# Performance work log

Measured on AMD Instinct MI355X. Metric: run time of the kernel, lower is better.

## Reference

```python
import jax, jax.numpy as jnp
import numpy as np

# ---- static config (mirrors init_kwargs) ----
B, T, N, FIN = 32, 12, 500, 2
U, ND, ED = 32, 32, 2            # factor dim, node_dim, edge_dim
NRES, NDIL, NSKIP, NEND, NPRED = 32, 32, 256, 512, 12
NBLOCKS, NLAYERS, KS, ORDER = 4, 2, 2, 2
L = NBLOCKS * NLAYERS
DILATIONS = [2 ** i for _ in range(NBLOCKS) for i in range(NLAYERS)]
RF = NBLOCKS * (KS - 1) * (2 ** NLAYERS - 1) + 1  # receptive field = 13
GCIN = (ORDER * ED + 1) * NDIL                     # graph-conv concat channels = 160
BN_EPS = 1e-5


def conv1x1(x, w, b):
    # x: [B,C,N,T], w: [O,C]
    return jnp.einsum('bcnt,oc->bont', x, w) + b[None, :, None, None]


def dilated_tconv(x, w, b, d):
    # valid dilated conv along time. x: [B,C,N,T], w: [O,C,K]
    k_sz = w.shape[-1]
    t_out = x.shape[-1] - (k_sz - 1) * d
    out = jnp.einsum('bcnt,oc->bont', x[..., 0:t_out], w[..., 0])
    for k in range(1, k_sz):
        out = out + jnp.einsum('bcnt,oc->bont', x[..., k * d:k * d + t_out], w[..., k])
    return out + b[None, :, None, None]


def graph_conv(x, supports, w, b):
    # x: [B,C,N,T]; supports: [E,N,N]; diffusion over node axis (dim 2)
    out = [x]
    for e in range(supports.shape[0]):
        x1 = jnp.einsum('bcvt,vw->bcwt', x, supports[e])
        out.append(x1)
        for _ in range(ORDER - 1):
            x1 = jnp.einsum('bcvt,vw->bcwt', x1, supports[e])
            out.append(x1)
    h = jnp.concatenate(out, axis=1)  # [B,GCIN,N,T]
    return conv1x1(h, w, b)


def batchnorm(x, g, bta):
    m = x.mean(axis=(0, 2, 3), keepdims=True)
    v = ((x - m) ** 2).mean(axis=(0, 2, 3), keepdims=True)
    return (x - m) * jax.lax.rsqrt(v + BN_EPS) * g[None, :, None, None] + bta[None, :, None, None]


def _forward(inputs, factor, map_w, map_b, a1w, a1b, a2w, a2b, a3w, a3b,
             enter_w, enter_b, filt_w, filt_b, gate_w, gate_b,
             skp_w, skp_b, gc_w, gc_b, bn_g, bn_b, o1w, o1b, o2w, o2b):
    n = factor.shape[0]
    # ---- adaptive supports ----
    v = jax.nn.relu(factor @ map_w + map_b)                      # [N, ND]
    src = jnp.broadcast_to(v[None, :, :], (n, n, v.shape[1]))    # src[i,j]=v[j]
    dst = jnp.broadcast_to(v[:, None, :], (n, n, v.shape[1]))    # dst[i,j]=v[i]
    h = jnp.concatenate([src, dst], axis=-1)                     # [N,N,2*ND]
    h = jax.nn.relu(h @ a1w + a1b)
    h = jax.nn.relu(h @ a2w + a2b)
    adj = (h @ a3w + a3b).transpose(2, 0, 1)                     # [E,N,N]
    adj = jax.nn.softmax(adj, axis=2)
    supports = jnp.maximum(adj, jnp.eye(n, dtype=adj.dtype))
    # ---- input split ----
    static = jnp.einsum('btuf,pu->btpf', jnp.einsum('btnf,nu->btuf', inputs, factor), factor)
    x = jnp.concatenate([static, inputs - static], axis=-1)      # [B,T,N,2F]
    x = x.transpose(0, 3, 2, 1)                                  # [B,2F,N,T]
    t_in = x.shape[-1]
    if t_in < RF:
        x = jnp.pad(x, ((0, 0), (0, 0), (0, 0), (RF - t_in, 0)))
    x = conv1x1(x, enter_w, enter_b)                             # [B,NRES,N,RF]
    skip = jnp.zeros((x.shape[0], NSKIP, n, x.shape[-1]), dtype=x.dtype)
    # ---- stacked ST layers ----
    for i, d in enumerate(DILATIONS):
        residual = x
        f = jnp.tanh(dilated_tconv(x, filt_w[i], filt_b[i], d))
        g = jax.nn.sigmoid(dilated_tconv(x, gate_w[i], gate_b[i], d))
        x = f * g                                                # [B,NDIL,N,T']
        s = conv1x1(x, skp_w[i], skp_b[i])
        skip = skip[..., skip.shape[-1] - s.shape[-1]:] + s
        x = graph_conv(x, supports, gc_w[i], gc_b[i])
        x = x + residual[..., residual.shape[-1] - x.shape[-1]:]
        x = batchnorm(x, bn_g[i], bn_b[i])
    # ---- output head ----
    y = jax.nn.relu(skip)
    y = jax.nn.relu(conv1x1(y, o1w, o1b))
    y = conv1x1(y, o2w, o2b)                                     # [B,NPRED,N,1]
    return y, supports


def setup_inputs() -> dict:
    key = jax.random.key(0)
    ks = jax.random.split(key, 16)
    def w(i, shape, s=0.02):
        return s * jax.random.normal(ks[i], shape, dtype=jnp.float32)
    return {
        'inputs': jax.random.normal(ks[0], (B, T, N, FIN), dtype=jnp.float32),
        'factor': 0.05 * jax.random.normal(ks[1], (N, U), dtype=jnp.float32),
        'map_w': w(2, (U, ND), 0.1), 'map_b': jnp.zeros((ND,), jnp.float32),
        'a1w': w(3, (2 * ND, 2 * ND), 0.1), 'a1b': jnp.zeros((2 * ND,), jnp.float32),
        'a2w': w(4, (2 * ND, ND), 0.1), 'a2b': jnp.zeros((ND,), jnp.float32),
        'a3w': w(5, (ND, ED), 0.1), 'a3b': jnp.zeros((ED,), jnp.float32),
        'enter_w': w(6, (NRES, 2 * FIN)), 'enter_b': jnp.zeros((NRES,), jnp.float32),
        'filt_w': w(7, (L, NDIL, NRES, KS)), 'filt_b': jnp.zeros((L, NDIL), jnp.float32),
        'gate_w': w(8, (L, NDIL, NRES, KS)), 'gate_b': jnp.zeros((L, NDIL), jnp.float32),
        'skp_w': w(9, (L, NSKIP, NDIL)), 'skp_b': jnp.zeros((L, NSKIP), jnp.float32),
        'gc_w': w(10, (L, NRES, GCIN)), 'gc_b': jnp.zeros((L, NRES), jnp.float32),
        'bn_g': jnp.ones((L, NRES), jnp.float32), 'bn_b': jnp.zeros((L, NRES), jnp.float32),
        'o1w': w(11, (NEND, NSKIP)), 'o1b': jnp.zeros((NEND,), jnp.float32),
        'o2w': w(12, (NPRED, NEND)), 'o2b': jnp.zeros((NPRED,), jnp.float32),
    }


def reference(inputs, factor, map_w, map_b, a1w, a1b, a2w, a2b, a3w, a3b,
              enter_w, enter_b, filt_w, filt_b, gate_w, gate_b,
              skp_w, skp_b, gc_w, gc_b, bn_g, bn_b, o1w, o1b, o2w, o2b):
    return _forward(inputs, factor, map_w, map_b, a1w, a1b, a2w, a2b, a3w, a3b,
                    enter_w, enter_b, filt_w, filt_b, gate_w, gate_b,
                    skp_w, skp_b, gc_w, gc_b, bn_g, bn_b, o1w, o1b, o2w, o2b)
```

## Files before the change

### kernel.cpp

```cpp
#include <hip/hip_runtime.h>
#include <math.h>

#define BB 32
#define TT 12
#define NN 500
#define UU 32
#define CC 32
#define NSKIPC 256
#define NENDC 512
#define NPREDC 12
#define TX 13
#define TG 12
#define QS 384
#define VS 512
#define BNN (BB*NN)
#define DSZ (BNN*TG*CC)
#define BN_EPS 1e-5f

#define OFF_V      0u
#define OFF_ADJ    16000u
#define OFF_ASRC   516000u
#define OFF_ADST   548000u
#define OFF_PROJ   580000u
#define OFF_STAT   582048u
#define OFF_PART   582560u
#define OFF_BSUM   774560u
#define OFF_X      774816u
#define OFF_XN     7430816u
#define OFF_D      14086816u
#define OFF_GBF    38662816u
#define OFF_GLB    41734816u
#define OFF_GT     43782816u
#define OFF_ST     46928544u
#define OFF_SB     47190688u
#define OFF_ST2    47452832u
#define OFF_WSTB   47714976u
#define OFF_O1WB   47747744u
#define OFF_SKV    47813280u
#define OFF_Y1B    49861280u

typedef __attribute__((ext_vector_type(8))) short bf16x8;
typedef __attribute__((ext_vector_type(4))) float f32x4;

__device__ inline unsigned short f2bf(float f) {
  union { float f; unsigned u; } x; x.f = f;
  unsigned r = x.u + 0x7FFFu + ((x.u >> 16) & 1u);
  return (unsigned short)(r >> 16);
}
__device__ inline float bf2f(short s) {
  union { float f; unsigned u; } x;
  x.u = ((unsigned)(unsigned short)s) << 16;
  return x.f;
}
__device__ inline int pk2(float a, float b) {
  return (int)((unsigned)f2bf(a) | ((unsigned)f2bf(b) << 16));
}
__device__ inline bf16x8 pack8(f32x4 a, f32x4 b) {
  union { int i[4]; bf16x8 v; } u;
  u.i[0]=pk2(a.x,a.y); u.i[1]=pk2(a.z,a.w);
  u.i[2]=pk2(b.x,b.y); u.i[3]=pk2(b.z,b.w);
  return u.v;
}
__device__ inline f32x4 reluadd(f32x4 a, f32x4 b) {
  f32x4 r;
  r.x=fmaxf(a.x+b.x,0.f); r.y=fmaxf(a.y+b.y,0.f);
  r.z=fmaxf(a.z+b.z,0.f); r.w=fmaxf(a.w+b.w,0.f);
  return r;
}


__global__ void k_v(const float* __restrict__ factor, const float* __restrict__ map_w,
                    const float* __restrict__ map_b, float* __restrict__ v) {
  int n = blockIdx.x; int d = threadIdx.x;
  __shared__ float fr[UU];
  fr[d] = factor[n*UU + d];
  __syncthreads();
  float acc = map_b[d];
#pragma unroll
  for (int u=0;u<UU;u++) acc += fr[u]*map_w[u*32+d];
  v[n*32+d] = fmaxf(acc, 0.f);
}

__global__ void k_asrc2(const float* __restrict__ v, const float* __restrict__ a1w,
                        const float* __restrict__ a1b,
                        float* __restrict__ asrc, float* __restrict__ adst) {
  int n = blockIdx.x; int o = threadIdx.x;
  __shared__ float vn[32];
  if (o < 32) vn[o] = v[n*32+o];
  __syncthreads();
  float s = 0.f, dst = a1b[o];
#pragma unroll
  for (int u=0;u<32;u++){ s += vn[u]*a1w[u*64+o]; dst += vn[u]*a1w[(32+u)*64+o]; }
  asrc[n*64+o] = s;
  adst[n*64+o] = dst;
}

__global__ __launch_bounds__(256) void k_pair3(const float* __restrict__ asrc,
    const float* __restrict__ adst, const float* __restrict__ a2w,
    const float* __restrict__ a2b, const float* __restrict__ a3w,
    const float* __restrict__ a3b, float* __restrict__ adj) {
  int i = blockIdx.x;
  int tid = threadIdx.x;
  int wid = tid>>6, lane = tid&63;
  int lm = lane&15, g = lane>>4, lk8 = g*8;
  int jb = blockIdx.y*256 + wid*64;
  bf16x8 wf[2][2];
#pragma unroll
  for (int ks=0;ks<2;ks++)
#pragma unroll
    for (int nh=0;nh<2;nh++){
      int n = nh*16+lm;
      f32x4 lo, hi;
      lo.x=a2w[(ks*32+lk8+0)*32+n]; lo.y=a2w[(ks*32+lk8+1)*32+n];
      lo.z=a2w[(ks*32+lk8+2)*32+n]; lo.w=a2w[(ks*32+lk8+3)*32+n];
      hi.x=a2w[(ks*32+lk8+4)*32+n]; hi.y=a2w[(ks*32+lk8+5)*32+n];
      hi.z=a2w[(ks*32+lk8+6)*32+n]; hi.w=a2w[(ks*32+lk8+7)*32+n];
      wf[ks][nh] = pack8(lo, hi);
    }
  float b20 = a2b[lm], b21 = a2b[16+lm];
  float w3e0n0 = a3w[lm*2],      w3e1n0 = a3w[lm*2+1];
  float w3e0n1 = a3w[(16+lm)*2], w3e1n1 = a3w[(16+lm)*2+1];
  float b30 = a3b[0], b31 = a3b[1];
  const float* dp = adst + i*64;
  f32x4 d00 = *(const f32x4*)(dp + lk8);
  f32x4 d01 = *(const f32x4*)(dp + lk8 + 4);
  f32x4 d10 = *(const f32x4*)(dp + 32 + lk8);
  f32x4 d11 = *(const f32x4*)(dp + 32 + lk8 + 4);
#pragma unroll
  for (int mg=0; mg<4; mg++){
    int j = jb + mg*16 + lm;
    int jc = j < 500 ? j : 0;
    const float* ap = asrc + jc*64;
    f32x4 s00=*(const f32x4*)(ap+lk8),    s01=*(const f32x4*)(ap+lk8+4);
    f32x4 s10=*(const f32x4*)(ap+32+lk8), s11=*(const f32x4*)(ap+32+lk8+4);
    bf16x8 a0 = pack8(reluadd(s00,d00), reluadd(s01,d01));
    bf16x8 a1 = pack8(reluadd(s10,d10), reluadd(s11,d11));
    f32x4 acc0 = {b20,b20,b20,b20};
    f32x4 acc1 = {b21,b21,b21,b21};
    acc0 = __builtin_amdgcn_mfma_f32_16x16x32_bf16(a0, wf[0][0], acc0, 0,0,0);
    acc0 = __builtin_amdgcn_mfma_f32_16x16x32_bf16(a1, wf[1][0], acc0, 0,0,0);
    acc1 = __builtin_amdgcn_mfma_f32_16x16x32_bf16(a0, wf[0][1], acc1, 0,0,0);
    acc1 = __builtin_amdgcn_mfma_f32_16x16x32_bf16(a1, wf[1][1], acc1, 0,0,0);
    float e0[4], e1[4];
#pragma unroll
    for (int r=0;r<4;r++){
      float h2a = fmaxf(acc0[r],0.f), h2b = fmaxf(acc1[r],0.f);
      e0[r] = h2a*w3e0n0 + h2b*w3e0n1;
      e1[r] = h2a*w3e1n0 + h2b*w3e1n1;
    }
#pragma unroll
    for (int off=1; off<16; off<<=1){
#pragma unroll
      for (int r=0;r<4;r++){ e0[r]+=__shfl_xor(e0[r],off); e1[r]+=__shfl_xor(e1[r],off); }
    }
    if (lm==0){
      int j4 = jb + mg*16 + g*4;
      if (j4 < 500){
        f32x4 v0={e0[0]+b30,e0[1]+b30,e0[2]+b30,e0[3]+b30};
        f32x4 v1={e1[0]+b31,e1[1]+b31,e1[2]+b31,e1[3]+b31};
        *(f32x4*)(adj + i*500 + j4) = v0;
        *(f32x4*)(adj + 250000 + i*500 + j4) = v1;
      }
    }
  }
}

__global__ __launch_bounds__(256) void k_softmax(const float* __restrict__ adj,
    float* __restrict__ sup_out) {
  int row = blockIdx.x;
  int e = row/NN, i = row%NN;
  const float* a = adj + e*250000 + i*NN;
  __shared__ float red[64];
  float m = -1e30f;
  for (int j=threadIdx.x;j<NN;j+=256) m = fmaxf(m, a[j]);
#pragma unroll
  for (int off=32; off; off>>=1) m = fmaxf(m, __shfl_down(m, off));
  int lane = threadIdx.x & 63, wid = threadIdx.x >> 6;
  if (lane==0) red[wid]=m;
  __syncthreads();
  if (threadIdx.x==0){ float mm=red[0]; for(int w=1;w<4;w++) mm=fmaxf(mm,red[w]); red[32]=mm; }
  __syncthreads();
  m = red[32];
  float s=0.f;
  for (int j=threadIdx.x;j<NN;j+=256) s += __expf(a[j]-m);
#pragma unroll
  for (int off=32; off; off>>=1) s += __shfl_down(s, off);
  if (lane==0) red[wid]=s;
  __syncthreads();
  if (threadIdx.x==0){ float ss=0; for(int w=0;w<4;w++) ss+=red[w]; red[33]=ss; }
  __syncthreads();
  float inv = 1.f/red[33];
  for (int j=threadIdx.x;j<NN;j+=256) {
    float val = __expf(a[j]-m)*inv;
    if (j==i) val = 1.f;
    sup_out[e*250000 + i*NN + j] = val;
  }
}

__global__ __launch_bounds__(256) void k_tposeS(const float* __restrict__ sup,
    short* __restrict__ ST, short* __restrict__ SB) {
  __shared__ float ts[64][68];
  int e = blockIdx.z;
  int v0 = blockIdx.x*64, w0 = blockIdx.y*64;
  int tid = threadIdx.x;
  int vv = tid>>2, wc = (tid&3)*16;
  bool vok = (v0+vv) < 500;
#pragma unroll
  for (int c=0;c<4;c++){
    f32x4 val = {0,0,0,0};
    int wg = w0 + wc + c*4;
    if (vok && wg < 500) val = *(const f32x4*)(sup + e*250000 + (size_t)(v0+vv)*500 + wg);
    *(f32x4*)&ts[vv][wc + c*4] = val;
    int2 pv; pv.x = pk2(val.x, val.y); pv.y = pk2(val.z, val.w);
    *(int2*)(SB + (size_t)e*(512*512) + (size_t)(v0+vv)*VS + wg) = pv;
  }
  __syncthreads();
  int w = tid>>2, vc = (tid&3)*16;
  unsigned short u[16];
#pragma unroll
  for (int j=0;j<16;j++) u[j] = f2bf(ts[vc+j][w]);
  int4 o0, o1;
  o0.x = u[0]|(u[1]<<16);  o0.y = u[2]|(u[3]<<16);
  o0.z = u[4]|(u[5]<<16);  o0.w = u[6]|(u[7]<<16);
  o1.x = u[8]|(u[9]<<16);  o1.y = u[10]|(u[11]<<16);
  o1.z = u[12]|(u[13]<<16); o1.w = u[14]|(u[15]<<16);
  short* op = ST + (size_t)e*(512*512) + (size_t)(w0+w)*VS + v0 + vc;
  *(int4*)(op) = o0;
  *(int4*)(op+8) = o1;
}

__global__ __launch_bounds__(256) void k_ssq(const short* __restrict__ SB,
    const short* __restrict__ ST, short* __restrict__ ST2) {
  __shared__ __align__(16) short As[64*72];
  __shared__ __align__(16) short Bs[64*72];
  int e = blockIdx.z;
  int u0 = blockIdx.x*64, w0 = blockIdx.y*64;
  const short* Ab = SB + (size_t)e*(512*512);
  const short* Bb = ST + (size_t)e*(512*512);
  int tid = threadIdx.x;
  int row = tid>>2, col = (tid&3)*16;
  const short* ap = Ab + (size_t)(u0+row)*VS + col;
  const short* bp = Bb + (size_t)(w0+row)*VS + col;
  f32x4 ra0 = *(const f32x4*)(ap);
  f32x4 ra1 = *(const f32x4*)(ap+8);
  f32x4 rb0 = *(const f32x4*)(bp);
  f32x4 rb1 = *(const f32x4*)(bp+8);
  int wid = tid>>6, lane = tid&63;
  int wr = wid>>1, wc = wid&1;
  int lm = lane&15, lk = (lane>>4)*8;
  f32x4 acc[2][2] = {};
  short* aw = As + row*72 + col;
  short* bw = Bs + row*72 + col;
  for (int kk=0; kk<8; kk++) {
    __syncthreads();
    *(f32x4*)(aw) = ra0; *(f32x4*)(aw+8) = ra1;
    *(f32x4*)(bw) = rb0; *(f32x4*)(bw+8) = rb1;
    __syncthreads();
    if (kk < 7) {
      const short* ap2 = ap + (kk+1)*64;
      const short* bp2 = bp + (kk+1)*64;
      ra0 = *(const f32x4*)(ap2); ra1 = *(const f32x4*)(ap2+8);
      rb0 = *(const f32x4*)(bp2); rb1 = *(const f32x4*)(bp2+8);
    }
#pragma unroll
    for (int ks=0; ks<2; ks++) {
      bf16x8 af0 = *(const bf16x8*)(As + (wr*32 + lm)*72 + ks*32 + lk);
      bf16x8 af1 = *(const bf16x8*)(As + (wr*32 + 16 + lm)*72 + ks*32 + lk);
      bf16x8 bq0 = *(const bf16x8*)(Bs + (wc*32 + lm)*72 + ks*32 + lk);
      bf16x8 bq1 = *(const bf16x8*)(Bs + (wc*32 + 16 + lm)*72 + ks*32 + lk);
      acc[0][0] = __builtin_amdgcn_mfma_f32_16x16x32_bf16(af0, bq0, acc[0][0], 0,0,0);
      acc[0][1] = __builtin_amdgcn_mfma_f32_16x16x32_bf16(af0, bq1, acc[0][1], 0,0,0);
      acc[1][0] = __builtin_amdgcn_mfma_f32_16x16x32_bf16(af1, bq0, acc[1][0], 0,0,0);
      acc[1][1] = __builtin_amdgcn_mfma_f32_16x16x32_bf16(af1, bq1, acc[1][1], 0,0,0);
    }
  }
#pragma unroll
  for (int fm=0; fm<2; fm++) {
    int u4 = u0 + wr*32 + fm*16 + (lane>>4)*4;
#pragma unroll
    for (int fn=0; fn<2; fn++) {
      int w = w0 + wc*32 + fn*16 + lm;
      f32x4 v4 = acc[fm][fn];
      int2 pv; pv.x = pk2(v4.x, v4.y); pv.y = pk2(v4.z, v4.w);
      *(int2*)(ST2 + (size_t)e*(512*512) + (size_t)w*VS + u4) = pv;
    }
  }
}

__global__ __launch_bounds__(256) void k_tposeGb(const short* __restrict__ Gbf,
    short* __restrict__ GT, int qmax) {
  __shared__ __align__(16) short ts[64][72];
  int b = blockIdx.z;
  int v0 = blockIdx.x*64, q0 = blockIdx.y*64;
  int tid = threadIdx.x;
  int vv = tid>>2, qc = (tid&3)*16;
  bool ok = ((v0+vv) < 500) && ((q0+qc) < qmax);
  int4 z4 = {0,0,0,0};
  int4 i0 = z4, i1 = z4;
  if (ok){
    const short* gp = Gbf + (size_t)(b*NN + v0+vv)*QS + q0 + qc;
    i0 = *(const int4*)(gp);
    i1 = *(const int4*)(gp+8);
  }
  *(int4*)&ts[vv][qc] = i0;
  *(int4*)&ts[vv][qc+8] = i1;
  __syncthreads();
  int q = tid>>2, vc = (tid&3)*16;
  if (q0 + q < qmax) {
    unsigned short u[16];
#pragma unroll
    for (int j=0;j<16;j++) u[j] = (unsigned short)ts[vc+j][q];
    int4 o0, o1;
    o0.x = u[0]|(u[1]<<16);  o0.y = u[2]|(u[3]<<16);
    o0.z = u[4]|(u[5]<<16);  o0.w = u[6]|(u[7]<<16);
    o1.x = u[8]|(u[9]<<16);  o1.y = u[10]|(u[11]<<16);
    o1.z = u[12]|(u[13]<<16); o1.w = u[14]|(u[15]<<16);
    short* op = GT + ((size_t)b*QS + q0+q)*VS + v0 + vc;
    *(int4*)(op) = o0;
    *(int4*)(op+8) = o1;
  }
}

__global__ __launch_bounds__(256) void k_hop2(const short* __restrict__ ST,
    const short* __restrict__ ST2, const short* __restrict__ GT,
    short* __restrict__ Dout, int qmax) {
  __shared__ __align__(16) short As[128*72];
  __shared__ __align__(16) short Bs[128*72];
  int sel = blockIdx.z & 3, b = blockIdx.z >> 2;
  int e = sel >> 1, hop = sel & 1;
  int w0 = blockIdx.x*128, q0 = blockIdx.y*128;
  const short* Ab = (hop ? ST2 : ST) + (size_t)e*(512*512) + (size_t)w0*VS;
  const short* Bb = GT + (size_t)b*(QS*VS) + (size_t)q0*VS;
  int tid = threadIdx.x;
  int row = tid>>2, col = (tid&3)*16;
  const short* ap0 = Ab + (size_t)row*VS + col;
  const short* ap1 = ap0 + (size_t)64*VS;
  const short* bp0 = Bb + (size_t)row*VS + col;
  const short* bp1 = bp0 + (size_t)64*VS;
  f32x4 a00=*(const f32x4*)ap0, a01=*(const f32x4*)(ap0+8);
  f32x4 a10=*(const f32x4*)ap1, a11=*(const f32x4*)(ap1+8);
  f32x4 b00=*(const f32x4*)bp0, b01=*(const f32x4*)(bp0+8);
  f32x4 b10=*(const f32x4*)bp1, b11=*(const f32x4*)(bp1+8);
  int wid = tid>>6, lane = tid&63;
  int wr = wid>>1, wc = wid&1;
  int lm = lane&15, lk = (lane>>4)*8;
  f32x4 acc[4][4] = {};
  short* aw0 = As + row*72 + col; short* aw1 = aw0 + 64*72;
  short* bw0 = Bs + row*72 + col; short* bw1 = bw0 + 64*72;
  for (int kk=0; kk<8; kk++) {
    __syncthreads();
    *(f32x4*)(aw0) = a00; *(f32x4*)(aw0+8) = a01;
    *(f32x4*)(aw1) = a10; *(f32x4*)(aw1+8) = a11;
    *(f32x4*)(bw0) = b00; *(f32x4*)(bw0+8) = b01;
    *(f32x4*)(bw1) = b10; *(f32x4*)(bw1+8) = b11;
    __syncthreads();
    if (kk < 7) {
      int o = (kk+1)*64;
      a00=*(const f32x4*)(ap0+o); a01=*(const f32x4*)(ap0+o+8);
      a10=*(const f32x4*)(ap1+o); a11=*(const f32x4*)(ap1+o+8);
      b00=*(const f32x4*)(bp0+o); b01=*(const f32x4*)(bp0+o+8);
      b10=*(const f32x4*)(bp1+o); b11=*(const f32x4*)(bp1+o+8);
    }
#pragma unroll
    for (int ks=0; ks<2; ks++) {
      bf16x8 af[4], bq[4];
#pragma unroll
      for (int fm=0;fm<4;fm++) af[fm] = *(const bf16x8*)(As + (wr*64+fm*16+lm)*72 + ks*32 + lk);
#pragma unroll
      for (int fn=0;fn<4;fn++) bq[fn] = *(const bf16x8*)(Bs + (wc*64+fn*16+lm)*72 + ks*32 + lk);
#pragma unroll
      for (int fm=0;fm<4;fm++)
#pragma unroll
        for (int fn=0;fn<4;fn++)
          acc[fm][fn] = __builtin_amdgcn_mfma_f32_16x16x32_bf16(af[fm], bq[fn], acc[fm][fn], 0,0,0);
    }
  }
  short* Ob = Dout + (size_t)sel*DSZ + (size_t)b*(NN*QS);
#pragma unroll
  for (int fm=0; fm<4; fm++) {
    int wb4 = w0 + wr*64 + fm*16 + (lane>>4)*4;
    if (wb4 >= 500) continue;
#pragma unroll
    for (int fn=0; fn<4; fn++) {
      int q = q0 + wc*64 + fn*16 + lm;
      if (q < qmax) {
        f32x4 v4 = acc[fm][fn];
        short* op = Ob + (size_t)wb4*QS + q;
        op[0*QS] = (short)f2bf(v4.x);
        op[1*QS] = (short)f2bf(v4.y);
        op[2*QS] = (short)f2bf(v4.z);
        op[3*QS] = (short)f2bf(v4.w);
      }
    }
  }
}


__global__ void k_proj(const float* __restrict__ inputs, const float* __restrict__ factor,
                       float* __restrict__ proj) {
  int bt = blockIdx.x;
  __shared__ float xin[NN*2];
  for (int idx=threadIdx.x; idx<NN*2; idx+=64) xin[idx] = inputs[bt*NN*2 + idx];
  __syncthreads();
  int u = threadIdx.x>>1, f = threadIdx.x&1;
  float acc=0.f;
  for (int n=0;n<NN;n++) acc += xin[n*2+f]*factor[n*UU+u];
  proj[bt*64 + u*2+f] = acc;
}

__global__ __launch_bounds__(256) void k_enter(const float* __restrict__ inputs,
    const float* __restrict__ factor, const float* __restrict__ proj,
    const float* __restrict__ ew, const float* __restrict__ eb, float* __restrict__ X) {
  int idx = blockIdx.x*256+threadIdx.x;
  if (idx >= BB*NN*TX) return;
  int t = idx % TX; int n = (idx/TX)%NN; int b = idx/(TX*NN);
  float x4[4]={0.f,0.f,0.f,0.f};
  if (t>0) {
    int tt=t-1;
    float s0=0.f,s1=0.f;
    const float* pr = proj + (b*TT+tt)*64;
    const float* fr = factor + n*UU;
#pragma unroll
    for(int u=0;u<UU;u++){ s0 += pr[u*2]*fr[u]; s1 += pr[u*2+1]*fr[u]; }
    float i0 = inputs[((b*TT+tt)*NN+n)*2];
    float i1 = inputs[((b*TT+tt)*NN+n)*2+1];
    x4[0]=s0; x4[1]=s1; x4[2]=i0-s0; x4[3]=i1-s1;
  }
  float* xp = X + ((size_t)(b*NN+n)*TX + t)*CC;
#pragma unroll
  for(int o=0;o<CC;o++){
    xp[o] = eb[o] + ew[o*4]*x4[0] + ew[o*4+1]*x4[1] + ew[o*4+2]*x4[2] + ew[o*4+3]*x4[3];
  }
}


__global__ __launch_bounds__(256) void k_gated3(const float* __restrict__ X,
    short* __restrict__ Gbf, short* __restrict__ Glb,
    const float* __restrict__ fw, const float* __restrict__ fb,
    const float* __restrict__ gw, const float* __restrict__ gb,
    const float* __restrict__ stat, int use_stat, int d, int t_out, int lidx) {
  __shared__ __align__(16) short As[64*72];
  __shared__ __align__(16) short Wb[64*72];
  __shared__ float scs[32], shs[32];
  int tid = threadIdx.x;
  if (tid < 32) {
    scs[tid] = use_stat ? stat[tid] : 1.0f;
    shs[tid] = use_stat ? stat[32 + tid] : 0.0f;
  }
  for (int i = tid; i < 2048; i += 256) {
    int o = i >> 6, k = i & 63;
    Wb[o*72 + k]      = (short)f2bf(fw[i]);
    Wb[(32+o)*72 + k] = (short)f2bf(gw[i]);
  }
  __syncthreads();
  int m0 = blockIdx.x * 64;
  {
    int mm = tid & 63;
    int kb = (tid >> 6) * 16;
    int c0 = kb >> 1;
    int m = m0 + mm;
    int bn = m / t_out, t = m - bn * t_out;
    const float* xr = X + (size_t)bn * (TX * CC);
    float4 a0 = *(const float4*)(xr + t * 32 + c0);
    float4 a1 = *(const float4*)(xr + t * 32 + c0 + 4);
    float4 b0 = *(const float4*)(xr + (t + d) * 32 + c0);
    float4 b1 = *(const float4*)(xr + (t + d) * 32 + c0 + 4);
    float va[8] = {a0.x,a0.y,a0.z,a0.w,a1.x,a1.y,a1.z,a1.w};
    float vb[8] = {b0.x,b0.y,b0.z,b0.w,b1.x,b1.y,b1.z,b1.w};
    int iv[8];
#pragma unroll
    for (int j = 0; j < 8; j++) {
      float sc = scs[c0+j], sh = shs[c0+j];
      iv[j] = pk2(va[j]*sc + sh, vb[j]*sc + sh);
    }
    int4 w0 = {iv[0],iv[1],iv[2],iv[3]};
    int4 w1 = {iv[4],iv[5],iv[6],iv[7]};
    *(int4*)(As + mm*72 + kb) = w0;
    *(int4*)(As + mm*72 + kb + 8) = w1;
  }
  __syncthreads();
  int wid = tid>>6, lane = tid&63;
  int lm = lane&15, g = lane>>4, lk8 = g*8;
  f32x4 acc[4] = {};
#pragma unroll
  for (int kk=0; kk<2; kk++){
    bf16x8 af = *(const bf16x8*)(As + (wid*16+lm)*72 + kk*32 + lk8);
#pragma unroll
    for (int fn=0; fn<4; fn++){
      bf16x8 bq = *(const bf16x8*)(Wb + (fn*16+lm)*72 + kk*32 + lk8);
      acc[fn] = __builtin_amdgcn_mfma_f32_16x16x32_bf16(af, bq, acc[fn], 0,0,0);
    }
  }
#pragma unroll
  for (int fn=0; fn<2; fn++){
    int o = fn*16 + lm;
    float fbv = fb[o], gbv = gb[o];
#pragma unroll
    for (int r=0; r<4; r++){
      int m = m0 + wid*16 + g*4 + r;
      int bn = m / t_out, t = m - bn*t_out;
      float f = acc[fn][r] + fbv;
      float gg = acc[fn+2][r] + gbv;
      float th = 2.f/(1.f+__expf(-2.f*f)) - 1.f;
      float sg = 1.f/(1.f+__expf(-gg));
      unsigned short ov = f2bf(th*sg);
      Gbf[(size_t)bn*QS + t*32 + o] = (short)ov;
      if (t == t_out-1) Glb[(size_t)bn*256 + lidx*32 + o] = (short)ov;
    }
  }
}


template<int TOUT>
__global__ __launch_bounds__(256) void k_gc3(const short* __restrict__ Gbf,
    const short* __restrict__ Dbf, const float* __restrict__ Xc, float* __restrict__ Xn,
    const float* __restrict__ gcw, const float* __restrict__ gcb,
    const float* __restrict__ stat, int use_stat, float* __restrict__ part, int d) {
  int tid = threadIdx.x;
  int wid = tid>>6, lane = tid&63;
  int lm = lane&15, g = lane>>4, lk8 = g*8;
  int m0 = blockIdx.x*256 + wid*64;
  const int M = 16000*TOUT;
  float* pp = part + ((size_t)blockIdx.x*4 + wid)*64;
  if (m0 >= M){
    if (lane < 16){ pp[lane]=0.f; pp[16+lane]=0.f; pp[32+lane]=0.f; pp[48+lane]=0.f; }
    return;
  }
  bf16x8 wf[5][2];
#pragma unroll
  for (int ks=0;ks<5;ks++)
#pragma unroll
    for (int nh=0;nh<2;nh++){
      const float* wp = gcw + (nh*16+lm)*160 + ks*32 + lk8;
      wf[ks][nh] = pack8(*(const f32x4*)wp, *(const f32x4*)(wp+4));
    }
  float scn0 = use_stat ? stat[lm]    : 1.f;
  float scn1 = use_stat ? stat[16+lm] : 1.f;
  float shn0 = use_stat ? stat[32+lm] : 0.f;
  float shn1 = use_stat ? stat[48+lm] : 0.f;
  float gb0 = gcb[lm], gb1 = gcb[16+lm];
  float ss0=0.f, sq0=0.f, ss1=0.f, sq1=0.f;
#pragma unroll
  for (int mg=0; mg<4; mg++){
    int m = m0 + mg*16 + lm;
    int bn = m / TOUT; int t = m - bn*TOUT;
    size_t off = (size_t)bn*(TG*CC) + t*32 + lk8;
    f32x4 acc0={0,0,0,0}, acc1={0,0,0,0};
    {
      bf16x8 af = *(const bf16x8*)(Gbf + off);
      acc0 = __builtin_amdgcn_mfma_f32_16x16x32_bf16(af, wf[0][0], acc0, 0,0,0);
      acc1 = __builtin_amdgcn_mfma_f32_16x16x32_bf16(af, wf[0][1], acc1, 0,0,0);
    }
#pragma unroll
    for (int ks=1;ks<5;ks++){
      bf16x8 af = *(const bf16x8*)(Dbf + (size_t)(ks-1)*DSZ + off);
      acc0 = __builtin_amdgcn_mfma_f32_16x16x32_bf16(af, wf[ks][0], acc0, 0,0,0);
      acc1 = __builtin_amdgcn_mfma_f32_16x16x32_bf16(af, wf[ks][1], acc1, 0,0,0);
    }
#pragma unroll
    for (int r=0;r<4;r++){
      int mr = m0 + mg*16 + g*4 + r;
      int bnr = mr / TOUT; int tr = mr - bnr*TOUT;
      size_t xoff = (size_t)bnr*(TX*CC);
      float r0 = Xc[xoff + (tr+d)*32 + lm];
      float r1 = Xc[xoff + (tr+d)*32 + 16 + lm];
      float v0 = acc0[r] + gb0 + r0*scn0 + shn0;
      float v1 = acc1[r] + gb1 + r1*scn1 + shn1;
      Xn[xoff + tr*32 + lm] = v0;
      Xn[xoff + tr*32 + 16 + lm] = v1;
      ss0+=v0; sq0+=v0*v0; ss1+=v1; sq1+=v1*v1;
    }
  }
#pragma unroll
  for (int off=16; off<64; off<<=1){
    ss0+=__shfl_xor(ss0,off); sq0+=__shfl_xor(sq0,off);
    ss1+=__shfl_xor(ss1,off); sq1+=__shfl_xor(sq1,off);
  }
  if (lane<16){
    pp[lane]=ss0; pp[16+lane]=ss1; pp[32+lane]=sq0; pp[48+lane]=sq1;
  }
}

__global__ __launch_bounds__(64) void k_stat2a(const float* __restrict__ part, int nblk,
    float* __restrict__ part2) {
  int t = threadIdx.x;
  float s = 0.f;
  for (int i = blockIdx.x; i < nblk; i += 64) s += part[(size_t)i*64 + t];
  part2[blockIdx.x*64 + t] = s;
}

__global__ __launch_bounds__(64) void k_stat2b(const float* __restrict__ part2,
    const float* __restrict__ g, const float* __restrict__ b,
    float* __restrict__ statout, float cntinv) {
  int t = threadIdx.x;
  float s = 0.f;
#pragma unroll 8
  for (int i = 0; i < 64; i++) s += part2[i*64 + t];
  __shared__ float red[64];
  red[t] = s;
  __syncthreads();
  if (t < 32){
    float sum = red[t], sq = red[32+t];
    float m = sum*cntinv, var = sq*cntinv - m*m;
    float sc = rsqrtf(var + BN_EPS)*g[t];
    statout[t] = sc;
    statout[32+t] = b[t] - m*sc;
  }
}


__global__ void k_wstack2(const float* __restrict__ skp_w, const float* __restrict__ skp_b,
                          const float* __restrict__ o1w,
                          short* __restrict__ Wstb, short* __restrict__ o1wb,
                          float* __restrict__ bsum) {
  int bid = blockIdx.x;
  int idx = bid*256 + threadIdx.x;
  if (bid < 256){
    int kk = idx >> 8, o = idx & 255;
    Wstb[o*256 + kk] = (short)f2bf(skp_w[(kk>>5)*8192 + o*32 + (kk&31)]);
    if (idx < 256){
      float s=0.f;
      for (int l=0;l<8;l++) s += skp_b[l*256+idx];
      bsum[idx]=s;
    }
  } else {
    int j = idx - 65536;
    o1wb[j] = (short)f2bf(o1w[j]);
  }
}

__global__ __launch_bounds__(256) void k_mm(const short* __restrict__ A,
    const short* __restrict__ B, const float* __restrict__ bias,
    short* __restrict__ out, int ldout, int K) {
  __shared__ __align__(16) short As[64*72];
  __shared__ __align__(16) short Bs[64*72];
  int m0 = blockIdx.x*64, n0 = blockIdx.y*64;
  int tid = threadIdx.x;
  int row = tid>>2, col = (tid&3)*16;
  const short* ap = A + (size_t)(m0+row)*K + col;
  const short* bp = B + (size_t)(n0+row)*K + col;
  f32x4 ra0 = *(const f32x4*)(ap);
  f32x4 ra1 = *(const f32x4*)(ap+8);
  f32x4 rb0 = *(const f32x4*)(bp);
  f32x4 rb1 = *(const f32x4*)(bp+8);
  int wid = tid>>6, lane = tid&63;
  int wr = wid>>1, wc = wid&1;
  int lm = lane&15, lk = (lane>>4)*8;
  f32x4 acc[2][2] = {};
  short* aw = As + row*72 + col;
  short* bw = Bs + row*72 + col;
  int nk = K>>6;
  for (int kk=0; kk<nk; kk++) {
    __syncthreads();
    *(f32x4*)(aw) = ra0; *(f32x4*)(aw+8) = ra1;
    *(f32x4*)(bw) = rb0; *(f32x4*)(bw+8) = rb1;
    __syncthreads();
    if (kk < nk-1) {
      const short* ap2 = ap + (kk+1)*64;
      const short* bp2 = bp + (kk+1)*64;
      ra0 = *(const f32x4*)(ap2); ra1 = *(const f32x4*)(ap2+8);
      rb0 = *(const f32x4*)(bp2); rb1 = *(const f32x4*)(bp2+8);
    }
#pragma unroll
    for (int ks=0; ks<2; ks++) {
      bf16x8 af0 = *(const bf16x8*)(As + (wr*32 + lm)*72 + ks*32 + lk);
      bf16x8 af1 = *(const bf16x8*)(As + (wr*32 + 16 + lm)*72 + ks*32 + lk);
      bf16x8 bq0 = *(const bf16x8*)(Bs + (wc*32 + lm)*72 + ks*32 + lk);
      bf16x8 bq1 = *(const bf16x8*)(Bs + (wc*32 + 16 + lm)*72 + ks*32 + lk);
      acc[0][0] = __builtin_amdgcn_mfma_f32_16x16x32_bf16(af0, bq0, acc[0][0], 0,0,0);
      acc[0][1] = __builtin_amdgcn_mfma_f32_16x16x32_bf16(af0, bq1, acc[0][1], 0,0,0);
      acc[1][0] = __builtin_amdgcn_mfma_f32_16x16x32_bf16(af1, bq0, acc[1][0], 0,0,0);
      acc[1][1] = __builtin_amdgcn_mfma_f32_16x16x32_bf16(af1, bq1, acc[1][1], 0,0,0);
    }
  }
#pragma unroll
  for (int fm=0; fm<2; fm++) {
    int mb = m0 + wr*32 + fm*16 + (lane>>4)*4;
#pragma unroll
    for (int fn=0; fn<2; fn++) {
      int n = n0 + wc*32 + fn*16 + lm;
      float bv = bias[n];
      f32x4 v4 = acc[fm][fn];
#pragma unroll
      for (int r=0;r<4;r++)
        out[(size_t)(mb+r)*ldout + n] = (short)f2bf(fmaxf(v4[r]+bv, 0.f));
    }
  }
}

__global__ __launch_bounds__(256) void k_head2c(const short* __restrict__ Y1b,
    const float* __restrict__ o2w, const float* __restrict__ o2b, float* __restrict__ y) {
  int tid = threadIdx.x;
  int ml = tid>>2, kc = tid&3;
  int m = blockIdx.x*64 + ml;
  float accs[NPREDC] = {};
  for (int e=kc*128; e<kc*128+128; e+=8){
    bf16x8 yv = *(const bf16x8*)(Y1b + (size_t)m*NENDC + e);
    float yf[8];
#pragma unroll
    for (int j=0;j<8;j++) yf[j] = bf2f(yv[j]);
#pragma unroll
    for (int p=0;p<NPREDC;p++){
      const float* wp = o2w + p*NENDC + e;
      float a = 0.f;
#pragma unroll
      for (int j=0;j<8;j++) a += wp[j]*yf[j];
      accs[p] += a;
    }
  }
#pragma unroll
  for (int off=1; off<4; off<<=1)
#pragma unroll
    for (int p=0;p<NPREDC;p++) accs[p] += __shfl_xor(accs[p], off);
  if (kc==0){
    int b=m/NN, n=m%NN;
#pragma unroll
    for (int p=0;p<NPREDC;p++) y[(b*NPREDC+p)*NN+n] = accs[p] + o2b[p];
  }
}


extern "C" void kernel_launch(void* const* d_in, const int* in_sizes, int n_in,
                              void* d_out, int out_size, void* d_ws, size_t ws_size,
                              hipStream_t stream) {
  const float* inputs  = (const float*)d_in[0];
  const float* factor  = (const float*)d_in[1];
  const float* map_w   = (const float*)d_in[2];
  const float* map_b   = (const float*)d_in[3];
  const float* a1w     = (const float*)d_in[4];
  const float* a1b     = (const float*)d_in[5];
  const float* a2w     = (const float*)d_in[6];
  const float* a2b     = (const float*)d_in[7];
  const float* a3w     = (const float*)d_in[8];
  const float* a3b     = (const float*)d_in[9];
  const float* enter_w = (const float*)d_in[10];
  const float* enter_b = (const float*)d_in[11];
  const float* filt_w  = (const float*)d_in[12];
  const float* filt_b  = (const float*)d_in[13];
  const float* gate_w  = (const float*)d_in[14];
  const float* gate_b  = (const float*)d_in[15];
  const float* skp_w   = (const float*)d_in[16];
  const float* skp_b   = (const float*)d_in[17];
  const float* gc_w    = (const float*)d_in[18];
  const float* gc_b    = (const float*)d_in[19];
  const float* bn_g    = (const float*)d_in[20];
  const float* bn_b    = (const float*)d_in[21];
  const float* o1w     = (const float*)d_in[22];
  const float* o1b     = (const float*)d_in[23];
  const float* o2w     = (const float*)d_in[24];
  const float* o2b     = (const float*)d_in[25];
  (void)in_sizes; (void)n_in; (void)out_size; (void)ws_size;

  float* ws = (float*)d_ws;
  float* v      = ws + OFF_V;
  float* adj    = ws + OFF_ADJ;
  float* part2  = ws + OFF_ADJ;
  float* asrc   = ws + OFF_ASRC;
  float* adst   = ws + OFF_ADST;
  float* proj   = ws + OFF_PROJ;
  float* statb  = ws + OFF_STAT;
  float* part   = ws + OFF_PART;
  float* bsum   = ws + OFF_BSUM;
  float* X      = ws + OFF_X;
  float* Xn     = ws + OFF_XN;
  short* Dbf    = (short*)(ws + OFF_D);
  short* Gbf    = (short*)(ws + OFF_GBF);
  short* Glb    = (short*)(ws + OFF_GLB);
  short* GT     = (short*)(ws + OFF_GT);
  short* ST     = (short*)(ws + OFF_ST);
  short* SB     = (short*)(ws + OFF_SB);
  short* ST2    = (short*)(ws + OFF_ST2);
  short* Wstb   = (short*)(ws + OFF_WSTB);
  short* o1wb   = (short*)(ws + OFF_O1WB);
  short* skvb   = (short*)(ws + OFF_SKV);
  short* Y1b    = (short*)(ws + OFF_Y1B);

  float* y_out   = (float*)d_out;
  float* sup_out = y_out + BB*NPREDC*NN;

  k_v<<<NN, 32, 0, stream>>>(factor, map_w, map_b, v);
  k_asrc2<<<NN, 64, 0, stream>>>(v, a1w, a1b, asrc, adst);
  {
    dim3 gp(NN, 2);
    k_pair3<<<gp, 256, 0, stream>>>(asrc, adst, a2w, a2b, a3w, a3b, adj);
  }
  k_softmax<<<2*NN, 256, 0, stream>>>(adj, sup_out);
  {
    dim3 gt(8, 8, 2);
    k_tposeS<<<gt, 256, 0, stream>>>(sup_out, ST, SB);
    k_ssq<<<gt, 256, 0, stream>>>(SB, ST, ST2);
  }

  k_proj<<<BB*TT, 64, 0, stream>>>(inputs, factor, proj);
  k_enter<<<(BB*NN*TX+255)/256, 256, 0, stream>>>(inputs, factor, proj, enter_w, enter_b, X);

  k_wstack2<<<768, 256, 0, stream>>>(skp_w, skp_b, o1w, Wstb, o1wb, bsum);

  float* Xc = X; float* Xo = Xn;
  int t = TX;
  static const int dil[8]={1,2,1,2,1,2,1,2};
  for (int l=0;l<7;l++){
    int d=dil[l], t_out=t-d;
    const float* st = statb + (l>0 ? (l-1)*64 : 0);
    k_gated3<<<250*t_out,256,0,stream>>>(Xc, Gbf, Glb, filt_w + l*2048, filt_b + l*32,
                                         gate_w + l*2048, gate_b + l*32, st, l>0, d, t_out, l);
    int qmax = t_out*CC;
    int qt64 = (qmax+63)/64;
    dim3 gtp(8, qt64, 32);
    k_tposeGb<<<gtp,256,0,stream>>>(Gbf, GT, qmax);
    int qt128 = (qmax+127)/128;
    dim3 ghp(4, qt128, 128);
    k_hop2<<<ghp,256,0,stream>>>(ST, ST2, GT, Dbf, qmax);
    int nb = (16000*t_out + 255)/256;
    const float* gcwl = gc_w + l*5120;
    const float* gcbl = gc_b + l*32;
    switch (t_out){
      case 12: k_gc3<12><<<nb,256,0,stream>>>(Gbf,Dbf,Xc,Xo,gcwl,gcbl,st,l>0,part,d); break;
      case 10: k_gc3<10><<<nb,256,0,stream>>>(Gbf,Dbf,Xc,Xo,gcwl,gcbl,st,l>0,part,d); break;
      case  9: k_gc3< 9><<<nb,256,0,stream>>>(Gbf,Dbf,Xc,Xo,gcwl,gcbl,st,l>0,part,d); break;
      case  7: k_gc3< 7><<<nb,256,0,stream>>>(Gbf,Dbf,Xc,Xo,gcwl,gcbl,st,l>0,part,d); break;
      case  6: k_gc3< 6><<<nb,256,0,stream>>>(Gbf,Dbf,Xc,Xo,gcwl,gcbl,st,l>0,part,d); break;
      case  4: k_gc3< 4><<<nb,256,0,stream>>>(Gbf,Dbf,Xc,Xo,gcwl,gcbl,st,l>0,part,d); break;
      default: k_gc3< 3><<<nb,256,0,stream>>>(Gbf,Dbf,Xc,Xo,gcwl,gcbl,st,l>0,part,d); break;
    }
    k_stat2a<<<64,64,0,stream>>>(part, nb*4, part2);
    k_stat2b<<<1,64,0,stream>>>(part2, bn_g + l*32, bn_b + l*32,
                                statb + l*64, 1.f/(16000.f*(float)t_out));
    float* tmp=Xc; Xc=Xo; Xo=tmp;
    t = t_out;
  }
  k_gated3<<<250*1,256,0,stream>>>(Xc, Gbf, Glb, filt_w + 7*2048, filt_b + 7*32,
                                   gate_w + 7*2048, gate_b + 7*32, statb + 6*64, 1, 2, 1, 7);

  {
    dim3 gs(BNN/64, NSKIPC/64);
    k_mm<<<gs,256,0,stream>>>(Glb, Wstb, bsum, skvb, NSKIPC, 256);
    dim3 gh(BNN/64, NENDC/64);
    k_mm<<<gh,256,0,stream>>>(skvb, o1wb, o1b, Y1b, NENDC, 256);
    k_head2c<<<BNN/64,256,0,stream>>>(Y1b, o2w, o2b, y_out);
  }
}
```

Measured before the change: 771.4 us.

## Stage hop2 outputs through LDS, XCD-swizzle its grid, and use MFMA for head2

The k_hop2 epilogue now writes its bf16 accumulators into shared memory and then stores them to global as coalesced 16-byte rows, replacing scattered 2-byte stores. Its 3D grid is flattened to 1D, with a remapping that spreads consecutive blocks across the 8 XCDs to improve L2 locality. The scalar final head kernel becomes an MFMA kernel that packs the 12 prediction weights into bf16 fragments. Costs are an extra LDS round trip with two barriers, and the final projection weights are now rounded to bf16.

Measured after the change: 728.7 us. 1.06x faster.

```diff
diff --git a/kernel.cpp b/kernel.cpp
--- a/kernel.cpp
+++ b/kernel.cpp
@@ -323,12 +323,17 @@
 
 __global__ __launch_bounds__(256) void k_hop2(const short* __restrict__ ST,
     const short* __restrict__ ST2, const short* __restrict__ GT,
-    short* __restrict__ Dout, int qmax) {
-  __shared__ __align__(16) short As[128*72];
-  __shared__ __align__(16) short Bs[128*72];
-  int sel = blockIdx.z & 3, b = blockIdx.z >> 2;
+    short* __restrict__ Dout, int qmax, int qt) {
+  __shared__ __align__(16) short LB[2*128*72];
+  short* As = LB;
+  short* Bs = LB + 128*72;
+  int nwg = gridDim.x;
+  int w = (blockIdx.x & 7) * (nwg >> 3) + (blockIdx.x >> 3);
+  int x = w & 3; w >>= 2;
+  int y = w % qt; w /= qt;
+  int sel = w & 3; int b = w >> 2;
   int e = sel >> 1, hop = sel & 1;
-  int w0 = blockIdx.x*128, q0 = blockIdx.y*128;
+  int w0 = x*128, q0 = y*128;
   const short* Ab = (hop ? ST2 : ST) + (size_t)e*(512*512) + (size_t)w0*VS;
   const short* Bb = GT + (size_t)b*(QS*VS) + (size_t)q0*VS;
   int tid = threadIdx.x;
@@ -375,22 +380,30 @@
           acc[fm][fn] = __builtin_amdgcn_mfma_f32_16x16x32_bf16(af[fm], bq[fn], acc[fm][fn], 0,0,0);
     }
   }
+  __syncthreads();
+#pragma unroll
+  for (int fm=0; fm<4; fm++){
+    int rr = wr*64 + fm*16 + (lane>>4)*4;
+#pragma unroll
+    for (int fn=0; fn<4; fn++){
+      int cc = wc*64 + fn*16 + lm;
+      f32x4 v4 = acc[fm][fn];
+      LB[(rr+0)*136 + cc] = (short)f2bf(v4.x);
+      LB[(rr+1)*136 + cc] = (short)f2bf(v4.y);
+      LB[(rr+2)*136 + cc] = (short)f2bf(v4.z);
+      LB[(rr+3)*136 + cc] = (short)f2bf(v4.w);
+    }
+  }
+  __syncthreads();
   short* Ob = Dout + (size_t)sel*DSZ + (size_t)b*(NN*QS);
 #pragma unroll
-  for (int fm=0; fm<4; fm++) {
-    int wb4 = w0 + wr*64 + fm*16 + (lane>>4)*4;
-    if (wb4 >= 500) continue;
-#pragma unroll
-    for (int fn=0; fn<4; fn++) {
-      int q = q0 + wc*64 + fn*16 + lm;
-      if (q < qmax) {
-        f32x4 v4 = acc[fm][fn];
-        short* op = Ob + (size_t)wb4*QS + q;
-        op[0*QS] = (short)f2bf(v4.x);
-        op[1*QS] = (short)f2bf(v4.y);
-        op[2*QS] = (short)f2bf(v4.z);
-        op[3*QS] = (short)f2bf(v4.w);
-      }
+  for (int pass=0; pass<8; pass++){
+    int rr = pass*16 + (tid>>4);
+    int cc = (tid&15)*8;
+    int wg = w0 + rr, qg = q0 + cc;
+    if (wg < 500 && qg < qmax){
+      int4 vv = *(const int4*)(LB + rr*136 + cc);
+      *(int4*)(Ob + (size_t)wg*QS + qg) = vv;
     }
   }
 }
@@ -688,34 +701,38 @@
   }
 }
 
-__global__ __launch_bounds__(256) void k_head2c(const short* __restrict__ Y1b,
+__global__ __launch_bounds__(256) void k_head2m(const short* __restrict__ Y1b,
     const float* __restrict__ o2w, const float* __restrict__ o2b, float* __restrict__ y) {
   int tid = threadIdx.x;
-  int ml = tid>>2, kc = tid&3;
-  int m = blockIdx.x*64 + ml;
-  float accs[NPREDC] = {};
-  for (int e=kc*128; e<kc*128+128; e+=8){
-    bf16x8 yv = *(const bf16x8*)(Y1b + (size_t)m*NENDC + e);
-    float yf[8];
-#pragma unroll
-    for (int j=0;j<8;j++) yf[j] = bf2f(yv[j]);
-#pragma unroll
-    for (int p=0;p<NPREDC;p++){
-      const float* wp = o2w + p*NENDC + e;
-      float a = 0.f;
-#pragma unroll
-      for (int j=0;j<8;j++) a += wp[j]*yf[j];
-      accs[p] += a;
-    }
-  }
-#pragma unroll
-  for (int off=1; off<4; off<<=1)
-#pragma unroll
-    for (int p=0;p<NPREDC;p++) accs[p] += __shfl_xor(accs[p], off);
-  if (kc==0){
-    int b=m/NN, n=m%NN;
-#pragma unroll
-    for (int p=0;p<NPREDC;p++) y[(b*NPREDC+p)*NN+n] = accs[p] + o2b[p];
+  int wid = tid>>6, lane = tid&63;
+  int lm = lane&15, g = lane>>4, lk8 = g*8;
+  int m0 = blockIdx.x*64 + wid*16;
+  bf16x8 wf[16];
+#pragma unroll
+  for (int ks=0; ks<16; ks++){
+    f32x4 lo={0,0,0,0}, hi={0,0,0,0};
+    if (lm < NPREDC){
+      const float* wp = o2w + lm*NENDC + ks*32 + lk8;
+      lo = *(const f32x4*)wp; hi = *(const f32x4*)(wp+4);
+    }
+    wf[ks] = pack8(lo, hi);
+  }
+  f32x4 acc = {0,0,0,0};
+  const short* ar = Y1b + (size_t)(m0+lm)*NENDC;
+#pragma unroll
+  for (int ks=0; ks<16; ks++){
+    bf16x8 af = *(const bf16x8*)(ar + ks*32 + lk8);
+    acc = __builtin_amdgcn_mfma_f32_16x16x32_bf16(af, wf[ks], acc, 0,0,0);
+  }
+  int p = lm;
+  if (p < NPREDC){
+    float bv = o2b[p];
+#pragma unroll
+    for (int r=0;r<4;r++){
+      int m = m0 + g*4 + r;
+      int bb = m/NN, n = m - bb*NN;
+      y[(bb*NPREDC+p)*NN + n] = acc[r] + bv;
+    }
   }
 }
 
@@ -809,8 +826,7 @@
     dim3 gtp(8, qt64, 32);
     k_tposeGb<<<gtp,256,0,stream>>>(Gbf, GT, qmax);
     int qt128 = (qmax+127)/128;
-    dim3 ghp(4, qt128, 128);
-    k_hop2<<<ghp,256,0,stream>>>(ST, ST2, GT, Dbf, qmax);
+    k_hop2<<<512*qt128,256,0,stream>>>(ST, ST2, GT, Dbf, qmax, qt128);
     int nb = (16000*t_out + 255)/256;
     const float* gcwl = gc_w + l*5120;
     const float* gcbl = gc_b + l*32;
@@ -837,6 +853,6 @@
     k_mm<<<gs,256,0,stream>>>(Glb, Wstb, bsum, skvb, NSKIPC, 256);
     dim3 gh(BNN/64, NENDC/64);
     k_mm<<<gh,256,0,stream>>>(skvb, o1wb, o1b, Y1b, NENDC, 256);
-    k_head2c<<<BNN/64,256,0,stream>>>(Y1b, o2w, o2b, y_out);
-  }
-}
+    k_head2m<<<BNN/64,256,0,stream>>>(Y1b, o2w, o2b, y_out);
+  }
+}
```
